# Optimization experiments

Measured on AMD Instinct MI355X. Metric: run time of the kernel, lower is better.

Reference implementation:

```python
import jax, jax.numpy as jnp
import numpy as np
from jax import lax

HEADS = 4
DSTATE = 8
DHALF = 64
DTRANK = 8
GRID_SIZE = 5
SPLINE_ORDER = 3


def _ln(x, g, b, eps=1e-5):
    mu = x.mean(-1, keepdims=True)
    v = ((x - mu) ** 2).mean(-1, keepdims=True)
    return (x - mu) / jnp.sqrt(v + eps) * g + b


def _make_grid(in_f):
    h = 2.0 / GRID_SIZE
    g = jnp.arange(-SPLINE_ORDER, GRID_SIZE + SPLINE_ORDER + 1, dtype=jnp.float32) * h - 1.0
    return jnp.tile(g[None, :], (in_f, 1))  # (in, grid+2k+1)


def _b_splines(x, grid):
    # x: (batch, in); grid: (in, G+2k+1) -> (batch, in, G+k)
    xe = x[:, :, None]
    bases = ((xe >= grid[:, :-1]) & (xe < grid[:, 1:])).astype(x.dtype)
    for k in range(1, SPLINE_ORDER + 1):
        bases = ((xe - grid[:, :-(k + 1)]) / (grid[:, k:-1] - grid[:, :-(k + 1)])) * bases[:, :, :-1] \
              + ((grid[:, k + 1:] - xe) / (grid[:, k + 1:] - grid[:, 1:-k])) * bases[:, :, 1:]
    return bases


def _kan_layer(x, bw, sw, sc, grid):
    base = jax.nn.silu(x) @ bw.T
    bs = _b_splines(x, grid)
    return base + jnp.einsum('bic,oic->bo', bs, sw * sc[:, :, None])


def _fkan(x, ng, nb, bw0, sw0, sc0, bw1, sw1, sc1):
    B, N, C = x.shape
    xf = _ln(x, ng, nb).reshape(B * N, C)
    h = _kan_layer(xf, bw0, sw0, sc0, _make_grid(C))
    y = _kan_layer(h, bw1, sw1, sc1, _make_grid(bw0.shape[0]))
    return y.reshape(B, N, C)


def _conv1x1(x, w, b):
    return jnp.einsum('bchw,oc->bohw', x, w[:, :, 0, 0]) + b[None, :, None, None]


def _dwconv2d(x, w, b):
    y = lax.conv_general_dilated(x, w, (1, 1), 'SAME', feature_group_count=x.shape[1],
                                 dimension_numbers=('NCHW', 'OIHW', 'NCHW'))
    return y + b[None, :, None, None]


def _dwconv1d(x, w):
    return lax.conv_general_dilated(x, w, (1,), 'SAME', feature_group_count=x.shape[1],
                                    dimension_numbers=('NCH', 'OIH', 'NCH'))


def _attention(x, temp, qkv_w, qkv_b, dw_w, dw_b, po_w, po_b):
    b, c, h, w = x.shape
    qkv = _dwconv2d(_conv1x1(x, qkv_w, qkv_b), dw_w, dw_b)
    q, k, v = jnp.split(qkv, 3, axis=1)
    rs = lambda t: t.reshape(b, HEADS, c // HEADS, h * w)
    q, k, v = rs(q), rs(k), rs(v)
    q = q / jnp.maximum(jnp.linalg.norm(q, axis=-1, keepdims=True), 1e-12)
    k = k / jnp.maximum(jnp.linalg.norm(k, axis=-1, keepdims=True), 1e-12)
    attn = jax.nn.softmax(jnp.einsum('bhcn,bhdn->bhcd', q, k) * temp, axis=-1)
    out = jnp.einsum('bhcd,bhdn->bhcn', attn, v).reshape(b, c, h, w)
    return _conv1x1(out, po_w, po_b)


def _mamba(x, in_w, xp_w, dt_w, dt_b, A_log, Dp, out_w, cx_w, cz_w):
    B, L, C = x.shape
    xz = x @ in_w.T                       # (B, L, d_inner)
    xc, zc = jnp.split(xz, 2, axis=-1)    # each (B, L, DHALF)
    xl = jax.nn.silu(_dwconv1d(xc.transpose(0, 2, 1), cx_w)).transpose(0, 2, 1)
    zl = jax.nn.silu(_dwconv1d(zc.transpose(0, 2, 1), cz_w)).transpose(0, 2, 1)
    x_dbl = xl @ xp_w.T                   # (B, L, dt_rank + 2*d_state)
    dt, Bm, Cm = jnp.split(x_dbl, [DTRANK, DTRANK + DSTATE], axis=-1)
    delta = jax.nn.softplus(dt @ dt_w.T + dt_b)   # (B, L, DHALF)
    A = -jnp.exp(A_log)                   # (DHALF, DSTATE)
    dA = jnp.exp(jnp.einsum('bld,dn->bldn', delta, A))
    dBu = delta[..., None] * Bm[:, :, None, :] * xl[..., None]

    def step(hst, inp):
        dA_t, dBu_t, C_t = inp
        hst = dA_t * hst + dBu_t
        return hst, jnp.einsum('bdn,bn->bd', hst, C_t)

    h0 = jnp.zeros((B, DHALF, DSTATE), x.dtype)
    _, ys = lax.scan(step, h0, (dA.transpose(1, 0, 2, 3), dBu.transpose(1, 0, 2, 3), Cm.transpose(1, 0, 2)))
    y = ys.transpose(1, 0, 2) + xl * Dp
    return jnp.concatenate([y, zl], axis=-1) @ out_w.T


def _forward(x5d, ln1_g, ln1_b, ln2_g, ln2_b, ln3_g, ln3_b, ln4_g, ln4_b,
             attn_temp, attn_qkv_w, attn_qkv_b, attn_dw_w, attn_dw_b, attn_po_w, attn_po_b,
             ffn1_ng, ffn1_nb, ffn1_bw0, ffn1_sw0, ffn1_sc0, ffn1_bw1, ffn1_sw1, ffn1_sc1,
             ffn2_ng, ffn2_nb, ffn2_bw0, ffn2_sw0, ffn2_sc0, ffn2_bw1, ffn2_sw1, ffn2_sc1,
             in_proj_w, x_proj_w, dt_proj_w, dt_proj_b, A_log, D_param, out_proj_w, conv_x_w, conv_z_w):
    B, C, Dd, H, W = x5d.shape
    N = Dd * H * W
    Hs = int(np.sqrt(N))
    x = x5d.reshape(B, C, N).transpose(0, 2, 1)   # (B, N, C)
    t2d = _ln(x, ln1_g, ln1_b).transpose(0, 2, 1).reshape(B, C, Hs, Hs)
    a = _attention(t2d, attn_temp, attn_qkv_w, attn_qkv_b, attn_dw_w, attn_dw_b, attn_po_w, attn_po_b)
    t = x + a.reshape(B, C, N).transpose(0, 2, 1)
    u = _fkan(_ln(t, ln2_g, ln2_b), ffn1_ng, ffn1_nb, ffn1_bw0, ffn1_sw0, ffn1_sc0, ffn1_bw1, ffn1_sw1, ffn1_sc1) + t
    x_tr = x + u
    m = _mamba(_ln(x_tr, ln3_g, ln3_b), in_proj_w, x_proj_w, dt_proj_w, dt_proj_b, A_log, D_param, out_proj_w, conv_x_w, conv_z_w) + x_tr
    n = _fkan(_ln(m, ln4_g, ln4_b), ffn2_ng, ffn2_nb, ffn2_bw0, ffn2_sw0, ffn2_sc0, ffn2_bw1, ffn2_sw1, ffn2_sc1) + m
    out = x_tr + n
    return out.transpose(0, 2, 1).reshape(B, C, Dd, H, W)


def setup_inputs():
    key = jax.random.key(0)
    ks = iter(jax.random.split(key, 48))
    f32 = jnp.float32

    def rn(shape, s=0.05):
        return jax.random.normal(next(ks), shape, f32) * s

    B, C, Dd, H, W = 2, 128, 1, 96, 96
    MLP = 512
    d = {}
    d['x5d'] = jax.random.normal(next(ks), (B, C, Dd, H, W), f32)
    for nm in ('ln1', 'ln2', 'ln3', 'ln4'):
        d[nm + '_g'] = jnp.ones((C,), f32)
        d[nm + '_b'] = jnp.zeros((C,), f32)
    d['attn_temp'] = jnp.ones((HEADS, 1, 1), f32)
    d['attn_qkv_w'] = rn((3 * C, C, 1, 1)); d['attn_qkv_b'] = jnp.zeros((3 * C,), f32)
    d['attn_dw_w'] = rn((3 * C, 1, 3, 3), 0.2); d['attn_dw_b'] = jnp.zeros((3 * C,), f32)
    d['attn_po_w'] = rn((C, C, 1, 1)); d['attn_po_b'] = jnp.zeros((C,), f32)
    for p in ('ffn1', 'ffn2'):
        d[p + '_ng'] = jnp.ones((C,), f32); d[p + '_nb'] = jnp.zeros((C,), f32)
        d[p + '_bw0'] = rn((MLP, C)); d[p + '_sw0'] = rn((MLP, C, GRID_SIZE + SPLINE_ORDER), 0.02); d[p + '_sc0'] = jnp.ones((MLP, C), f32)
        d[p + '_bw1'] = rn((C, MLP)); d[p + '_sw1'] = rn((C, MLP, GRID_SIZE + SPLINE_ORDER), 0.02); d[p + '_sc1'] = jnp.ones((C, MLP), f32)
    d['in_proj_w'] = rn((C, C))
    d['x_proj_w'] = rn((DTRANK + 2 * DSTATE, DHALF))
    std = DTRANK ** -0.5
    d['dt_proj_w'] = jax.random.uniform(next(ks), (DHALF, DTRANK), f32, -std, std)
    dt = jnp.exp(jax.random.uniform(next(ks), (DHALF,), f32) * (np.log(0.1) - np.log(0.001)) + np.log(0.001))
    dt = jnp.clip(dt, 1e-4, None)
    d['dt_proj_b'] = dt + jnp.log(-jnp.expm1(-dt))
    d['A_log'] = jnp.log(jnp.tile(jnp.arange(1, DSTATE + 1, dtype=f32)[None, :], (DHALF, 1)))
    d['D_param'] = jnp.ones((DHALF,), f32)
    d['out_proj_w'] = rn((C, C))
    d['conv_x_w'] = rn((DHALF, 1, 3), 0.2)
    d['conv_z_w'] = rn((DHALF, 1, 3), 0.2)
    return d


def reference(x5d, ln1_g, ln1_b, ln2_g, ln2_b, ln3_g, ln3_b, ln4_g, ln4_b,
              attn_temp, attn_qkv_w, attn_qkv_b, attn_dw_w, attn_dw_b, attn_po_w, attn_po_b,
              ffn1_ng, ffn1_nb, ffn1_bw0, ffn1_sw0, ffn1_sc0, ffn1_bw1, ffn1_sw1, ffn1_sc1,
              ffn2_ng, ffn2_nb, ffn2_bw0, ffn2_sw0, ffn2_sc0, ffn2_bw1, ffn2_sw1, ffn2_sc1,
              in_proj_w, x_proj_w, dt_proj_w, dt_proj_b, A_log, D_param, out_proj_w, conv_x_w, conv_z_w):
    return _forward(x5d, ln1_g, ln1_b, ln2_g, ln2_b, ln3_g, ln3_b, ln4_g, ln4_b,
                    attn_temp, attn_qkv_w, attn_qkv_b, attn_dw_w, attn_dw_b, attn_po_w, attn_po_b,
                    ffn1_ng, ffn1_nb, ffn1_bw0, ffn1_sw0, ffn1_sc0, ffn1_bw1, ffn1_sw1, ffn1_sc1,
                    ffn2_ng, ffn2_nb, ffn2_bw0, ffn2_sw0, ffn2_sc0, ffn2_bw1, ffn2_sw1, ffn2_sc1,
                    in_proj_w, x_proj_w, dt_proj_w, dt_proj_b, A_log, D_param, out_proj_w, conv_x_w, conv_z_w)
```

## Files before the change

kernel.cpp:

```cpp
#include <hip/hip_runtime.h>

typedef unsigned short u16;
typedef __attribute__((ext_vector_type(8))) short bh8;
typedef __attribute__((ext_vector_type(4))) float f4;

#define DI __device__ __forceinline__

DI u16 f2bf(float f){ unsigned u=__float_as_uint(f); u += 0x7fffu + ((u>>16)&1u); return (u16)(u>>16); }
DI float bf2f(u16 u){ return __uint_as_float(((unsigned)u)<<16); }
DI float silu_f(float x){ return x/(1.f+__expf(-x)); }

DI void gld16(const u16* g, u16* l){
  __builtin_amdgcn_global_load_lds((const __attribute__((address_space(1))) void*)g,
                                   (__attribute__((address_space(3))) void*)l, 16, 0, 0);
}

DI void bspline8(float x, float* v){
  float u = x*2.5f + 5.5f;
  #pragma unroll
  for (int j=0;j<8;j++){
    float a  = fabsf(u - (float)(j+2));
    float t1 = fmaxf(2.f-a, 0.f);
    float t2 = fmaxf(1.f-a, 0.f);
    v[j] = t1*t1*t1*(1.f/6.f) - t2*t2*t2*(2.f/3.f);
  }
}

template<int KAN_H, bool OUT_BF16>
__global__ __launch_bounds__(256, 4)
void gemm_kernel(const void* __restrict__ Asrc, const u16* __restrict__ Bt,
                 void* __restrict__ Cout, int M, int N, int K, int ktiles_per_z,
                 int split, const float* __restrict__ bias, const float* __restrict__ R1)
{
  __shared__ u16 sA[128*64];
  __shared__ u16 sB[128*64];
  const int m0 = blockIdx.y * 128;
  const int n0 = blockIdx.x * 128;
  const int ktiles = K >> 6;
  int kt0 = blockIdx.z * ktiles_per_z;
  int kt1 = kt0 + ktiles_per_z; if (kt1 > ktiles) kt1 = ktiles;
  const int t = threadIdx.x;
  const int wave = t >> 6, lane = t & 63;
  const int wm = wave & 1, wn = wave >> 1;
  const int lr = lane & 15, lq = lane >> 4;
  const int lr8 = lane >> 3, lc8 = lane & 7;
  const int swz8 = lc8 ^ lr8;
  f4 acc[4][4];
  f4 z4 = {0.f,0.f,0.f,0.f};
  #pragma unroll
  for (int i=0;i<4;i++)
    #pragma unroll
    for (int j=0;j<4;j++) acc[i][j]=z4;

  for (int kt = kt0; kt < kt1; ++kt) {
    int k0 = kt << 6;
    {
      const u16* Bp = Bt + (size_t)n0 * K + k0;
      #pragma unroll
      for (int it=0; it<4; ++it) {
        int r = it*32 + wave*8;
        gld16(Bp + (size_t)(r + lr8) * K + swz8*8, &sB[r*64]);
      }
    }
    if (KAN_H == 0) {
      const u16* Ap = (const u16*)Asrc + (size_t)m0 * K + k0;
      #pragma unroll
      for (int it=0; it<4; ++it) {
        int r = it*32 + wave*8;
        gld16(Ap + (size_t)(r + lr8) * K + swz8*8, &sA[r*64]);
      }
    } else {
      const u16* hsrc = (const u16*)Asrc;
      if (k0 < KAN_H) {
        #pragma unroll
        for (int it=0; it<4; ++it) {
          int chunk = t + it*256;
          int r = chunk >> 3, ck = chunk & 7;
          const u16* src = hsrc + (size_t)(m0+r)*KAN_H + k0 + ck*8;
          ushort4 a = *(const ushort4*)src;
          ushort4 b2 = *(const ushort4*)(src+4);
          alignas(16) u16 o[8];
          o[0]=f2bf(silu_f(bf2f(a.x))); o[1]=f2bf(silu_f(bf2f(a.y)));
          o[2]=f2bf(silu_f(bf2f(a.z))); o[3]=f2bf(silu_f(bf2f(a.w)));
          o[4]=f2bf(silu_f(bf2f(b2.x))); o[5]=f2bf(silu_f(bf2f(b2.y)));
          o[6]=f2bf(silu_f(bf2f(b2.z))); o[7]=f2bf(silu_f(bf2f(b2.w)));
          *(float4*)(&sA[r*64 + (ck ^ (r&7))*8]) = *(const float4*)o;
        }
      } else {
        int i0 = (k0 - KAN_H) >> 3;
        #pragma unroll
        for (int it=0; it<4; ++it) {
          int chunk = t + it*256;
          int r = chunk >> 3, ii = chunk & 7;
          float x = bf2f(hsrc[(size_t)(m0+r)*KAN_H + i0 + ii]);
          float w[8];
          bspline8(x, w);
          alignas(16) u16 o[8];
          #pragma unroll
          for (int j=0;j<8;j++) o[j]=f2bf(w[j]);
          *(float4*)(&sA[r*64 + (ii ^ (r&7))*8]) = *(const float4*)o;
        }
      }
    }
    __syncthreads();
    #pragma unroll
    for (int kk=0; kk<64; kk+=32) {
      const int c0 = kk >> 3;
      bh8 af[4], bfr[4];
      #pragma unroll
      for (int i=0;i<4;i++) {
        int row = wm*64 + i*16 + lr;
        af[i] = *(const bh8*)(&sA[row*64 + ((c0+lq) ^ (row&7))*8]);
      }
      #pragma unroll
      for (int j=0;j<4;j++) {
        int row = wn*64 + j*16 + lr;
        bfr[j] = *(const bh8*)(&sB[row*64 + ((c0+lq) ^ (row&7))*8]);
      }
      #pragma unroll
      for (int i=0;i<4;i++)
        #pragma unroll
        for (int j=0;j<4;j++)
          acc[i][j] = __builtin_amdgcn_mfma_f32_16x16x32_bf16(af[i], bfr[j], acc[i][j], 0, 0, 0);
    }
    __syncthreads();
  }
  float* Cf = (float*)Cout;
  if (!OUT_BF16 && split) Cf += (size_t)blockIdx.z * M * N;
  u16* Cb = (u16*)Cout;
  #pragma unroll
  for (int i=0;i<4;i++) {
    int row = m0 + wm*64 + i*16 + lq*4;
    #pragma unroll
    for (int j=0;j<4;j++) {
      int col = n0 + wn*64 + j*16 + lr;
      float bv = bias ? bias[col] : 0.f;
      #pragma unroll
      for (int r4=0;r4<4;r4++) {
        size_t idx = (size_t)(row + r4) * N + col;
        float v = acc[i][j][r4] + bv;
        if (OUT_BF16) {
          Cb[idx] = f2bf(v);
        } else {
          if (R1) v += R1[idx];
          Cf[idx] = v;
        }
      }
    }
  }
}

__global__ __launch_bounds__(256) void k_ln1_trans(const float* __restrict__ x5d,
    float* __restrict__ x_t, u16* __restrict__ ln1_t,
    const float* __restrict__ g, const float* __restrict__ bv)
{
  __shared__ float tile[128*65];
  __shared__ float red_s[256], red_q[256];
  __shared__ float st_mu[64], st_rs[64];
  int b = blockIdx.y, n0 = blockIdx.x * 64;
  int j = threadIdx.x & 63, part = threadIdx.x >> 6;
  for (int cc=0; cc<32; ++cc) {
    int c = part*32 + cc;
    tile[c*65 + j] = x5d[((size_t)b*128 + c)*9216 + n0 + j];
  }
  __syncthreads();
  float s=0.f, s2=0.f;
  for (int cc=0; cc<32; ++cc) {
    float v = tile[(part*32+cc)*65 + j];
    s += v; s2 += v*v;
  }
  red_s[threadIdx.x]=s; red_q[threadIdx.x]=s2;
  __syncthreads();
  if (threadIdx.x < 64) {
    int jj = threadIdx.x;
    float ts = red_s[jj]+red_s[jj+64]+red_s[jj+128]+red_s[jj+192];
    float tq = red_q[jj]+red_q[jj+64]+red_q[jj+128]+red_q[jj+192];
    float mu = ts*(1.f/128.f);
    st_mu[jj]=mu;
    st_rs[jj]=rsqrtf(tq*(1.f/128.f) - mu*mu + 1e-5f);
  }
  __syncthreads();
  for (int it=0; it<32; ++it) {
    int idx = threadIdx.x + it*256;
    int tok = idx >> 7, c = idx & 127;
    float v = tile[c*65 + tok];
    size_t a = ((size_t)b*9216 + n0 + tok)*128 + c;
    x_t[a] = v;
    ln1_t[a] = f2bf((v - st_mu[tok])*st_rs[tok]*g[c] + bv[c]);
  }
}

__global__ void k_ln_bf16(const float* __restrict__ in, u16* __restrict__ out,
                          const float* __restrict__ g, const float* __restrict__ bv)
{
  int tok = blockIdx.x*4 + (threadIdx.x>>6);
  int lane = threadIdx.x & 63;
  const float* row = in + (size_t)tok*128;
  float v0=row[lane], v1=row[lane+64];
  float s=v0+v1, s2=v0*v0+v1*v1;
  #pragma unroll
  for (int o=1;o<64;o<<=1){ s += __shfl_xor(s,o); s2 += __shfl_xor(s2,o); }
  float mu=s*(1.f/128.f);
  float rs=rsqrtf(s2*(1.f/128.f)-mu*mu+1e-5f);
  u16* orow = out + (size_t)tok*128;
  orow[lane]    = f2bf((v0-mu)*rs*g[lane]+bv[lane]);
  orow[lane+64] = f2bf((v1-mu)*rs*g[lane+64]+bv[lane+64]);
}

__global__ void k_ln_double_expand(const float* __restrict__ in, u16* __restrict__ A1,
    const float* __restrict__ g1, const float* __restrict__ b1,
    const float* __restrict__ g2, const float* __restrict__ b2)
{
  int tok = blockIdx.x*4 + (threadIdx.x>>6);
  int lane = threadIdx.x & 63;
  const float* row = in + (size_t)tok*128;
  float v0=row[lane], v1=row[lane+64];
  float s=v0+v1, s2=v0*v0+v1*v1;
  #pragma unroll
  for (int o=1;o<64;o<<=1){ s += __shfl_xor(s,o); s2 += __shfl_xor(s2,o); }
  float mu=s*(1.f/128.f);
  float rs=rsqrtf(s2*(1.f/128.f)-mu*mu+1e-5f);
  float y0=(v0-mu)*rs*g1[lane]+b1[lane];
  float y1=(v1-mu)*rs*g1[lane+64]+b1[lane+64];
  s=y0+y1; s2=y0*y0+y1*y1;
  #pragma unroll
  for (int o=1;o<64;o<<=1){ s += __shfl_xor(s,o); s2 += __shfl_xor(s2,o); }
  mu=s*(1.f/128.f);
  rs=rsqrtf(s2*(1.f/128.f)-mu*mu+1e-5f);
  y0=(y0-mu)*rs*g2[lane]+b2[lane];
  y1=(y1-mu)*rs*g2[lane+64]+b2[lane+64];
  u16* arow = A1 + (size_t)tok*1152;
  arow[lane]    = f2bf(silu_f(y0));
  arow[lane+64] = f2bf(silu_f(y1));
  float w[8]; alignas(16) u16 o8[8];
  bspline8(y0, w);
  #pragma unroll
  for (int j=0;j<8;j++) o8[j]=f2bf(w[j]);
  *(float4*)(&arow[128 + lane*8]) = *(const float4*)o8;
  bspline8(y1, w);
  #pragma unroll
  for (int j=0;j<8;j++) o8[j]=f2bf(w[j]);
  *(float4*)(&arow[128 + (lane+64)*8]) = *(const float4*)o8;
}

__global__ __launch_bounds__(256) void k_dwconv(const u16* __restrict__ qkv_t,
    u16* __restrict__ qkvd, const float* __restrict__ dw_w, const float* __restrict__ dw_b)
{
  __shared__ float lt[100*68];
  int tile = blockIdx.x; int th=(tile/12)*8, tw=(tile%12)*8;
  int cg = blockIdx.y, b = blockIdx.z;
  int t = threadIdx.x;
  for (int pp=0; pp<7; ++pp) {
    int pos = pp*16 + (t>>4);
    if (pos < 100) {
      int ih = th + pos/10 - 1, iw = tw + pos%10 - 1;
      int c4 = (t & 15)*4;
      float4 v = make_float4(0.f,0.f,0.f,0.f);
      if (ih>=0 && ih<96 && iw>=0 && iw<96) {
        ushort4 raw = *(const ushort4*)&qkv_t[(((size_t)b*9216) + ih*96 + iw)*384 + cg*64 + c4];
        v = make_float4(bf2f(raw.x), bf2f(raw.y), bf2f(raw.z), bf2f(raw.w));
      }
      *(float4*)&lt[pos*68 + c4] = v;
    }
  }
  __syncthreads();
  int ch = t & 63, gch = cg*64 + ch;
  float w[9];
  #pragma unroll
  for (int k=0;k<9;k++) w[k]=dw_w[gch*9+k];
  float bias = dw_b[gch];
  for (int pp=0; pp<16; ++pp) {
    int pos = (t>>6) + pp*4;
    int oh = pos>>3, ow = pos&7;
    float acc = bias;
    #pragma unroll
    for (int di=0; di<3; ++di)
      #pragma unroll
      for (int dj=0; dj<3; ++dj)
        acc += lt[((oh+di)*10 + ow+dj)*68 + ch] * w[di*3+dj];
    qkvd[(((size_t)b*9216) + (th+oh)*96 + tw+ow)*384 + gch] = f2bf(acc);
  }
}

__global__ void k_normsum(const u16* __restrict__ qkvd, float* __restrict__ ss)
{
  int b = blockIdx.y, n0 = blockIdx.x*128;
  int c = threadIdx.x;
  float acc=0.f;
  for (int i=0;i<128;++i){
    float v = bf2f(qkvd[((size_t)b*9216 + n0+i)*384 + c]);
    acc += v*v;
  }
  atomicAdd(&ss[b*256 + c], acc);
}

__global__ __launch_bounds__(256) void k_qk(const u16* __restrict__ qkvd,
    const float* __restrict__ ss, float* __restrict__ S)
{
  __shared__ float ql[128][32];
  __shared__ float kl[128][32];
  int nc=blockIdx.x, h=blockIdx.y, b=blockIdx.z;
  int t = threadIdx.x;
  int r = t>>1, half = t&1;
  size_t rowa = ((size_t)b*9216 + nc*128 + r)*384 + (half?128:0) + h*32;
  #pragma unroll
  for (int cc=0; cc<32; ++cc) {
    float v = bf2f(qkvd[rowa + cc]);
    if (half) kl[r][cc]=v; else ql[r][cc]=v;
  }
  __syncthreads();
  int i0 = (t>>4)*2, j0 = (t&15)*2;
  float a00=0.f,a01=0.f,a10=0.f,a11=0.f;
  for (int n=0;n<128;++n){
    float2 qv = *(const float2*)&ql[n][i0];
    float2 kv = *(const float2*)&kl[n][j0];
    a00 += qv.x*kv.x; a01 += qv.x*kv.y;
    a10 += qv.y*kv.x; a11 += qv.y*kv.y;
  }
  const float* ssb = ss + b*256;
  float rq0 = 1.f/fmaxf(sqrtf(ssb[h*32+i0]),1e-12f);
  float rq1 = 1.f/fmaxf(sqrtf(ssb[h*32+i0+1]),1e-12f);
  float rk0 = 1.f/fmaxf(sqrtf(ssb[128+h*32+j0]),1e-12f);
  float rk1 = 1.f/fmaxf(sqrtf(ssb[128+h*32+j0+1]),1e-12f);
  float* Sp = S + ((size_t)(b*4+h))*1024;
  atomicAdd(&Sp[i0*32+j0],     a00*rq0*rk0);
  atomicAdd(&Sp[i0*32+j0+1],   a01*rq0*rk1);
  atomicAdd(&Sp[(i0+1)*32+j0], a10*rq1*rk0);
  atomicAdd(&Sp[(i0+1)*32+j0+1], a11*rq1*rk1);
}

__global__ void k_softmax(const float* __restrict__ S, float* __restrict__ attnP,
                          const float* __restrict__ temp)
{
  int bh = blockIdx.x; int h = bh & 3;
  int i = threadIdx.x;
  const float* row = S + (size_t)bh*1024 + i*32;
  float tp = temp[h];
  float vals[32]; float mx = -1e30f;
  #pragma unroll
  for (int j=0;j<32;++j){ float v=row[j]*tp; vals[j]=v; mx=fmaxf(mx,v); }
  float sum=0.f;
  #pragma unroll
  for (int j=0;j<32;++j){ vals[j]=__expf(vals[j]-mx); sum+=vals[j]; }
  float inv=1.f/sum;
  float* out = attnP + (size_t)bh*1024 + i*32;
  #pragma unroll
  for (int j=0;j<32;++j) out[j]=vals[j]*inv;
}

__global__ __launch_bounds__(256) void k_av(const u16* __restrict__ qkvd,
    const float* __restrict__ attnP, u16* __restrict__ attnout)
{
  __shared__ float at[1024];
  int b=blockIdx.z, h=blockIdx.y;
  int n = blockIdx.x*256 + threadIdx.x;
  #pragma unroll
  for (int it=0;it<4;++it)
    at[threadIdx.x + it*256] = attnP[((size_t)(b*4+h))*1024 + threadIdx.x + it*256];
  __syncthreads();
  const u16* vrow = &qkvd[((size_t)b*9216 + n)*384 + 256 + h*32];
  float acc[32];
  #pragma unroll
  for (int i=0;i<32;++i) acc[i]=0.f;
  #pragma unroll 4
  for (int j=0;j<32;++j){
    float vj = bf2f(vrow[j]);
    #pragma unroll
    for (int i=0;i<32;++i) acc[i] += at[i*32+j]*vj;
  }
  u16* orow = &attnout[((size_t)b*9216 + n)*128 + h*32];
  #pragma unroll
  for (int i=0;i<32;++i) orow[i] = f2bf(acc[i]);
}

__global__ void k_reduce4(const float4* __restrict__ P, const float4* __restrict__ R1,
                          const float4* __restrict__ R2, float4* __restrict__ o, int n4)
{
  int i = blockIdx.x*256 + threadIdx.x;
  if (i<n4){
    float4 a=P[i], b=P[i+n4], c=P[i+2*n4], d=P[i+3*n4], r=R1[i], s=R2[i];
    o[i]=make_float4(a.x+b.x+c.x+d.x+r.x+s.x, a.y+b.y+c.y+d.y+r.y+s.y,
                     a.z+b.z+c.z+d.z+r.z+s.z, a.w+b.w+c.w+d.w+r.w+s.w);
  }
}

__global__ void k_zero(float* p, int n){ int i=blockIdx.x*256+threadIdx.x; if(i<n)p[i]=0.f; }
__global__ void k_f2bf_copy(const float* __restrict__ in, u16* __restrict__ out, int n){
  int i=blockIdx.x*256+threadIdx.x; if(i<n) out[i]=f2bf(in[i]);
}

__global__ __launch_bounds__(256) void k_mamba_pre(const float* __restrict__ xz,
    float* __restrict__ xl, float* __restrict__ delta,
    float* __restrict__ Bm, float* __restrict__ Cm, u16* __restrict__ A_out,
    const float* __restrict__ cxw, const float* __restrict__ czw,
    const float* __restrict__ xpw, const float* __restrict__ dtw, const float* __restrict__ dtb)
{
  __shared__ float xls[4][64];
  __shared__ float xds[4][24];
  int w = threadIdx.x>>6;
  int tok = blockIdx.x*4 + w;
  int lane = threadIdx.x & 63;
  int l = tok % 9216;
  size_t base = (size_t)tok*128;
  float xm1 = (l>0)?     xz[base-128+lane]    : 0.f;
  float x0  =            xz[base+lane];
  float xp1 = (l<9215)?  xz[base+128+lane]    : 0.f;
  float zm1 = (l>0)?     xz[base-128+64+lane] : 0.f;
  float z0  =            xz[base+64+lane];
  float zp1 = (l<9215)?  xz[base+128+64+lane] : 0.f;
  float xc = silu_f(cxw[lane*3]*xm1 + cxw[lane*3+1]*x0 + cxw[lane*3+2]*xp1);
  float zc = silu_f(czw[lane*3]*zm1 + czw[lane*3+1]*z0 + czw[lane*3+2]*zp1);
  xl[(size_t)tok*64+lane] = xc;
  A_out[(size_t)tok*128 + 64 + lane] = f2bf(zc);
  xls[w][lane] = xc;
  __syncthreads();
  if (lane < 24) {
    float s=0.f;
    #pragma unroll 8
    for (int c=0;c<64;++c) s += xls[w][c]*xpw[lane*64+c];
    xds[w][lane]=s;
  }
  __syncthreads();
  float dacc = dtb[lane];
  #pragma unroll
  for (int r=0;r<8;++r) dacc += xds[w][r]*dtw[lane*8+r];
  delta[(size_t)tok*64+lane] = (dacc>20.f)? dacc : log1pf(__expf(dacc));
  if (lane<8)       Bm[(size_t)tok*8+lane]   = xds[w][8+lane];
  else if (lane<16) Cm[(size_t)tok*8+lane-8] = xds[w][16+lane-8];
}

__global__ __launch_bounds__(512) void k_scan1(const float* __restrict__ delta,
    const float* __restrict__ Bm, const float* __restrict__ xl,
    const float* __restrict__ Aneg, float* __restrict__ cP, float* __restrict__ cS)
{
  int b=blockIdx.y, ch=blockIdx.x;
  int t=threadIdx.x; int d=t>>3, n=t&7;
  float An = Aneg[d*8+n];
  float P=1.f, S=0.f;
  int l0 = ch*96;
  #pragma unroll 8
  for (int i=0;i<96;++i){
    size_t s = (size_t)b*9216 + l0+i;
    float del = delta[s*64+d];
    float a = __expf(del*An);
    float dbu = del * Bm[s*8+n] * xl[s*64+d];
    P *= a; S = fmaf(a,S,dbu);
  }
  size_t o = ((size_t)(b*96+ch))*512 + t;
  cP[o]=P; cS[o]=S;
}

__global__ __launch_bounds__(512) void k_scan2(const float* __restrict__ cP,
    const float* __restrict__ cS, float* __restrict__ cI)
{
  int b=blockIdx.x; int t=threadIdx.x;
  float carry=0.f;
  #pragma unroll 4
  for (int c=0;c<96;++c){
    size_t o = ((size_t)(b*96+c))*512 + t;
    cI[o]=carry;
    carry = fmaf(cP[o], carry, cS[o]);
  }
}

__global__ __launch_bounds__(512) void k_scan3(const float* __restrict__ delta,
    const float* __restrict__ Bm, const float* __restrict__ Cm,
    const float* __restrict__ xl, const float* __restrict__ Aneg,
    const float* __restrict__ Dp, const float* __restrict__ cI, u16* __restrict__ A_out)
{
  int b=blockIdx.y, ch=blockIdx.x;
  int t=threadIdx.x; int d=t>>3, n=t&7;
  float An = Aneg[d*8+n];
  float h = cI[((size_t)(b*96+ch))*512 + t];
  float Dd = Dp[d];
  int l0 = ch*96;
  #pragma unroll 4
  for (int i=0;i<96;++i){
    size_t s = (size_t)b*9216 + l0+i;
    float del = delta[s*64+d];
    float a = __expf(del*An);
    float xv = xl[s*64+d];
    h = fmaf(a, h, del * Bm[s*8+n] * xv);
    float contrib = h * Cm[s*8+n];
    contrib += __shfl_xor(contrib,1);
    contrib += __shfl_xor(contrib,2);
    contrib += __shfl_xor(contrib,4);
    if (n==0) A_out[s*128 + d] = f2bf(contrib + xv*Dd);
  }
}

__global__ __launch_bounds__(256) void k_transpose_out(const float* __restrict__ sfin,
                                                       float* __restrict__ out)
{
  __shared__ float tile[128*65];
  int b=blockIdx.y, n0=blockIdx.x*64;
  for (int it=0;it<32;++it){
    int idx = threadIdx.x + it*256;
    int tok = idx>>7, c = idx&127;
    tile[c*65+tok] = sfin[((size_t)b*9216 + n0+tok)*128 + c];
  }
  __syncthreads();
  int j = threadIdx.x & 63, part = threadIdx.x>>6;
  for (int cc=0;cc<32;++cc){
    int c = part*32+cc;
    out[((size_t)b*128 + c)*9216 + n0 + j] = tile[c*65 + j];
  }
}

__global__ void k_pack_w1t(const float* __restrict__ bw0, const float* __restrict__ sw0,
                           const float* __restrict__ sc0, u16* __restrict__ W1t)
{
  int idx = blockIdx.x*256 + threadIdx.x;
  if (idx >= 512*1152) return;
  int o = idx/1152, k = idx%1152;
  float v;
  if (k < 128) v = bw0[o*128+k];
  else { int i=(k-128)>>3, c=(k-128)&7; v = sw0[(o*128+i)*8+c]*sc0[o*128+i]; }
  W1t[idx]=f2bf(v);
}
__global__ void k_pack_w2t(const float* __restrict__ bw1, const float* __restrict__ sw1,
                           const float* __restrict__ sc1, u16* __restrict__ W2t)
{
  int idx = blockIdx.x*256 + threadIdx.x;
  if (idx >= 128*4608) return;
  int o = idx/4608, k = idx%4608;
  float v;
  if (k < 512) v = bw1[o*512+k];
  else { int i=(k-512)>>3, c=(k-512)&7; v = sw1[(o*512+i)*8+c]*sc1[o*512+i]; }
  W2t[idx]=f2bf(v);
}
__global__ void k_prep_aneg(const float* __restrict__ A_log, float* __restrict__ Aneg){
  int i=threadIdx.x; if (i<512) Aneg[i] = -__expf(A_log[i]);
}

extern "C" void kernel_launch(void* const* d_in, const int* in_sizes, int n_in,
                              void* d_out, int out_size, void* d_ws, size_t ws_size,
                              hipStream_t stream)
{
  (void)in_sizes; (void)n_in; (void)out_size; (void)ws_size;
  const float* x5d   =(const float*)d_in[0];
  const float* ln1_g =(const float*)d_in[1];
  const float* ln1_b =(const float*)d_in[2];
  const float* ln2_g =(const float*)d_in[3];
  const float* ln2_b =(const float*)d_in[4];
  const float* ln3_g =(const float*)d_in[5];
  const float* ln3_b =(const float*)d_in[6];
  const float* ln4_g =(const float*)d_in[7];
  const float* ln4_b =(const float*)d_in[8];
  const float* temp  =(const float*)d_in[9];
  const float* qkv_w =(const float*)d_in[10];
  const float* qkv_b =(const float*)d_in[11];
  const float* dw_w  =(const float*)d_in[12];
  const float* dw_b  =(const float*)d_in[13];
  const float* po_w  =(const float*)d_in[14];
  const float* po_b  =(const float*)d_in[15];
  const float* f1_ng =(const float*)d_in[16];
  const float* f1_nb =(const float*)d_in[17];
  const float* f1_bw0=(const float*)d_in[18];
  const float* f1_sw0=(const float*)d_in[19];
  const float* f1_sc0=(const float*)d_in[20];
  const float* f1_bw1=(const float*)d_in[21];
  const float* f1_sw1=(const float*)d_in[22];
  const float* f1_sc1=(const float*)d_in[23];
  const float* f2_ng =(const float*)d_in[24];
  const float* f2_nb =(const float*)d_in[25];
  const float* f2_bw0=(const float*)d_in[26];
  const float* f2_sw0=(const float*)d_in[27];
  const float* f2_sc0=(const float*)d_in[28];
  const float* f2_bw1=(const float*)d_in[29];
  const float* f2_sw1=(const float*)d_in[30];
  const float* f2_sc1=(const float*)d_in[31];
  const float* in_w  =(const float*)d_in[32];
  const float* xp_w  =(const float*)d_in[33];
  const float* dt_w  =(const float*)d_in[34];
  const float* dt_b  =(const float*)d_in[35];
  const float* A_log =(const float*)d_in[36];
  const float* Dp    =(const float*)d_in[37];
  const float* out_w =(const float*)d_in[38];
  const float* cx_w  =(const float*)d_in[39];
  const float* cz_w  =(const float*)d_in[40];
  float* out = (float*)d_out;

  const size_t T = 18432;
  char* wsb = (char*)d_ws;
  size_t off = 0;
  auto alloc = [&](size_t bytes)->void* {
    void* p = wsb + off; off += (bytes + 255) & ~(size_t)255; return p;
  };
  float* x_t    = (float*)alloc(T*128*4);
  char*  scrA   = (char*) alloc(38*1024*1024);
  float* ssS    = (float*)alloc((512+8192+8192)*4);
  float* t_t    = (float*)alloc(T*128*4);
  u16*   A1     = (u16*)  alloc(T*1152*2);
  u16*   hbuf   = (u16*)  alloc(T*512*2);
  float* xtr    = (float*)alloc(T*128*4);
  u16*   xm     = (u16*)  alloc(T*128*2);
  float* xl     = (float*)alloc(T*64*4);
  float* delta  = (float*)alloc(T*64*4);
  float* Bm     = (float*)alloc(T*8*4);
  float* Cm     = (float*)alloc(T*8*4);
  u16*   A_out  = (u16*)  alloc(T*128*2);
  float* cP     = (float*)alloc(2*96*512*4);
  float* cS     = (float*)alloc(2*96*512*4);
  float* cI     = (float*)alloc(2*96*512*4);
  float* sfin   = (float*)alloc(T*128*4);
  u16* qkvw_bf  = (u16*)alloc(384*128*2);
  u16* pow_bf   = (u16*)alloc(128*128*2);
  u16* inw_bf   = (u16*)alloc(128*128*2);
  u16* outw_bf  = (u16*)alloc(128*128*2);
  u16* W1t_a    = (u16*)alloc(512*1152*2);
  u16* W2t_a    = (u16*)alloc(128*4608*2);
  u16* W1t_b    = (u16*)alloc(512*1152*2);
  u16* W2t_b    = (u16*)alloc(128*4608*2);
  float* Aneg   = (float*)alloc(512*4);
  float* ss = ssS;
  float* S  = ssS + 512;
  float* attnP = ssS + 512 + 8192;
  u16*   ln1_t  = (u16*)(scrA);
  u16*   qkv_tb = (u16*)(scrA + 4718592);
  u16*   qkvd   = (u16*)(scrA + 4718592 + 14155776);
  u16*   attnout= (u16*)(scrA + 4718592 + 2*14155776);
  float* part   = (float*)scrA;
  float* xz     = (float*)scrA;
  float* m_t    = t_t;

  k_pack_w1t<<<2304,256,0,stream>>>(f1_bw0, f1_sw0, f1_sc0, W1t_a);
  k_pack_w1t<<<2304,256,0,stream>>>(f2_bw0, f2_sw0, f2_sc0, W1t_b);
  k_pack_w2t<<<2304,256,0,stream>>>(f1_bw1, f1_sw1, f1_sc1, W2t_a);
  k_pack_w2t<<<2304,256,0,stream>>>(f2_bw1, f2_sw1, f2_sc1, W2t_b);
  k_f2bf_copy<<<192,256,0,stream>>>(qkv_w, qkvw_bf, 384*128);
  k_f2bf_copy<<<64,256,0,stream>>>(po_w,  pow_bf, 128*128);
  k_f2bf_copy<<<64,256,0,stream>>>(in_w,  inw_bf, 128*128);
  k_f2bf_copy<<<64,256,0,stream>>>(out_w, outw_bf, 128*128);
  k_prep_aneg<<<1,512,0,stream>>>(A_log, Aneg);
  k_zero<<<34,256,0,stream>>>(ssS, 512+8192);

  k_ln1_trans<<<dim3(144,2),256,0,stream>>>(x5d, x_t, ln1_t, ln1_g, ln1_b);
  gemm_kernel<0,true><<<dim3(3,144,1),256,0,stream>>>(ln1_t, qkvw_bf, qkv_tb,
      18432, 384, 128, 2, 0, qkv_b, nullptr);
  k_dwconv<<<dim3(144,6,2),256,0,stream>>>(qkv_tb, qkvd, dw_w, dw_b);
  k_normsum<<<dim3(72,2),256,0,stream>>>(qkvd, ss);
  k_qk<<<dim3(72,4,2),256,0,stream>>>(qkvd, ss, S);
  k_softmax<<<8,32,0,stream>>>(S, attnP, temp);
  k_av<<<dim3(36,4,2),256,0,stream>>>(qkvd, attnP, attnout);
  gemm_kernel<0,false><<<dim3(1,144,1),256,0,stream>>>(attnout, pow_bf, t_t,
      18432, 128, 128, 2, 0, po_b, x_t);

  k_ln_double_expand<<<4608,256,0,stream>>>(t_t, A1, ln2_g, ln2_b, f1_ng, f1_nb);
  gemm_kernel<0,true><<<dim3(4,144,1),256,0,stream>>>(A1, W1t_a, hbuf,
      18432, 512, 1152, 18, 0, nullptr, nullptr);
  gemm_kernel<512,false><<<dim3(1,144,4),256,0,stream>>>(hbuf, W2t_a, part,
      18432, 128, 4608, 18, 1, nullptr, nullptr);
  k_reduce4<<<2304,256,0,stream>>>((const float4*)part, (const float4*)t_t,
      (const float4*)x_t, (float4*)xtr, (int)(T*128/4));

  k_ln_bf16<<<4608,256,0,stream>>>(xtr, xm, ln3_g, ln3_b);
  gemm_kernel<0,false><<<dim3(1,144,1),256,0,stream>>>(xm, inw_bf, xz,
      18432, 128, 128, 2, 0, nullptr, nullptr);
  k_mamba_pre<<<4608,256,0,stream>>>(xz, xl, delta, Bm, Cm, A_out,
      cx_w, cz_w, xp_w, dt_w, dt_b);
  k_scan1<<<dim3(96,2),512,0,stream>>>(delta, Bm, xl, Aneg, cP, cS);
  k_scan2<<<2,512,0,stream>>>(cP, cS, cI);
  k_scan3<<<dim3(96,2),512,0,stream>>>(delta, Bm, Cm, xl, Aneg, Dp, cI, A_out);
  gemm_kernel<0,false><<<dim3(1,144,1),256,0,stream>>>(A_out, outw_bf, m_t,
      18432, 128, 128, 2, 0, nullptr, xtr);

  k_ln_double_expand<<<4608,256,0,stream>>>(m_t, A1, ln4_g, ln4_b, f2_ng, f2_nb);
  gemm_kernel<0,true><<<dim3(4,144,1),256,0,stream>>>(A1, W1t_b, hbuf,
      18432, 512, 1152, 18, 0, nullptr, nullptr);
  gemm_kernel<512,false><<<dim3(1,144,4),256,0,stream>>>(hbuf, W2t_b, part,
      18432, 128, 4608, 18, 1, nullptr, nullptr);
  k_reduce4<<<2304,256,0,stream>>>((const float4*)part, (const float4*)m_t,
      (const float4*)xtr, (float4*)sfin, (int)(T*128/4));

  k_transpose_out<<<dim3(144,2),256,0,stream>>>(sfin, out);
}
```

Before: 593.5 us.

## Halve GEMM M-tile, sparsify spline basis, fuse reduce+LN and prep kernels

The GEMM tile shrinks from 128x128 to 64x128 and the grid's M dimension doubles from 144 to 288 blocks, giving more blocks across the GPU's CUs. The B-spline A-tile fill now computes only the 4 nonzero cubic weights, placed at their knot offset after zeroing the row, instead of evaluating all 8 bases. The residual reduction is fused with LayerNorm3, and the small weight-conversion, Aneg and zeroing kernels merge into one prep launch. The trade-off is less B-tile reuse per block, since each B tile loaded into shared memory now serves only 64 rows of A.

```diff
diff --git a/kernel.cpp b/kernel.cpp
--- a/kernel.cpp
+++ b/kernel.cpp
@@ -28,29 +28,26 @@
 
 template<int KAN_H, bool OUT_BF16>
 __global__ __launch_bounds__(256, 4)
-void gemm_kernel(const void* __restrict__ Asrc, const u16* __restrict__ Bt,
-                 void* __restrict__ Cout, int M, int N, int K, int ktiles_per_z,
-                 int split, const float* __restrict__ bias, const float* __restrict__ R1)
-{
-  __shared__ u16 sA[128*64];
+void gemm64(const void* __restrict__ Asrc, const u16* __restrict__ Bt,
+            void* __restrict__ Cout, int M, int N, int K, int ktiles_per_z,
+            int split, const float* __restrict__ bias, const float* __restrict__ R1)
+{
+  __shared__ u16 sA[64*64 + 8];
   __shared__ u16 sB[128*64];
-  const int m0 = blockIdx.y * 128;
+  const int m0 = blockIdx.y * 64;
   const int n0 = blockIdx.x * 128;
   const int ktiles = K >> 6;
   int kt0 = blockIdx.z * ktiles_per_z;
   int kt1 = kt0 + ktiles_per_z; if (kt1 > ktiles) kt1 = ktiles;
   const int t = threadIdx.x;
   const int wave = t >> 6, lane = t & 63;
-  const int wm = wave & 1, wn = wave >> 1;
   const int lr = lane & 15, lq = lane >> 4;
   const int lr8 = lane >> 3, lc8 = lane & 7;
   const int swz8 = lc8 ^ lr8;
-  f4 acc[4][4];
+  f4 acc[4][2];
   f4 z4 = {0.f,0.f,0.f,0.f};
   #pragma unroll
-  for (int i=0;i<4;i++)
-    #pragma unroll
-    for (int j=0;j<4;j++) acc[i][j]=z4;
+  for (int i=0;i<4;i++){ acc[i][0]=z4; acc[i][1]=z4; }
 
   for (int kt = kt0; kt < kt1; ++kt) {
     int k0 = kt << 6;
@@ -65,7 +62,7 @@
     if (KAN_H == 0) {
       const u16* Ap = (const u16*)Asrc + (size_t)m0 * K + k0;
       #pragma unroll
-      for (int it=0; it<4; ++it) {
+      for (int it=0; it<2; ++it) {
         int r = it*32 + wave*8;
         gld16(Ap + (size_t)(r + lr8) * K + swz8*8, &sA[r*64]);
       }
@@ -73,7 +70,7 @@
       const u16* hsrc = (const u16*)Asrc;
       if (k0 < KAN_H) {
         #pragma unroll
-        for (int it=0; it<4; ++it) {
+        for (int it=0; it<2; ++it) {
           int chunk = t + it*256;
           int r = chunk >> 3, ck = chunk & 7;
           const u16* src = hsrc + (size_t)(m0+r)*KAN_H + k0 + ck*8;
@@ -88,39 +85,55 @@
         }
       } else {
         int i0 = (k0 - KAN_H) >> 3;
+        const float4 zf4 = make_float4(0.f,0.f,0.f,0.f);
         #pragma unroll
-        for (int it=0; it<4; ++it) {
-          int chunk = t + it*256;
-          int r = chunk >> 3, ii = chunk & 7;
+        for (int it=0; it<2; ++it) {
+          int pair = t + it*256;
+          int r = pair >> 3, ii = pair & 7;
+          int base = r*64 + (ii ^ (r&7))*8;
+          *(float4*)(&sA[base]) = zf4;
           float x = bf2f(hsrc[(size_t)(m0+r)*KAN_H + i0 + ii]);
-          float w[8];
-          bspline8(x, w);
-          alignas(16) u16 o[8];
+          float u = x*2.5f + 5.5f;
+          bool valid = (u >= 0.f) & (u < 11.f);
+          float uc = fminf(fmaxf(u, 0.f), 10.999f);
+          int m = (int)uc;
+          float tt = uc - (float)m;
+          float omt = 1.f - tt, t2 = tt*tt, t3 = t2*tt;
+          float w0 = omt*omt*omt*(1.f/6.f);
+          float w3 = t3*(1.f/6.f);
+          float w1 = 0.5f*t3 - t2 + (2.f/3.f);
+          float w2 = 1.f - w0 - w1 - w3;
+          float ws[4] = {w0, w1, w2, w3};
+          int c0 = m - 3;
           #pragma unroll
-          for (int j=0;j<8;j++) o[j]=f2bf(w[j]);
-          *(float4*)(&sA[r*64 + (ii ^ (r&7))*8]) = *(const float4*)o;
+          for (int j=0;j<4;j++){
+            int c = c0 + j;
+            bool ok = valid & ((unsigned)c < 8u);
+            int off = ok ? (base + c) : (64*64);
+            sA[off] = f2bf(ws[j]);
+          }
         }
       }
     }
     __syncthreads();
     #pragma unroll
     for (int kk=0; kk<64; kk+=32) {
-      const int c0 = kk >> 3;
-      bh8 af[4], bfr[4];
+      const int c0k = kk >> 3;
+      bh8 af[4], bfr[2];
       #pragma unroll
       for (int i=0;i<4;i++) {
-        int row = wm*64 + i*16 + lr;
-        af[i] = *(const bh8*)(&sA[row*64 + ((c0+lq) ^ (row&7))*8]);
+        int row = i*16 + lr;
+        af[i] = *(const bh8*)(&sA[row*64 + ((c0k+lq) ^ (row&7))*8]);
       }
       #pragma unroll
-      for (int j=0;j<4;j++) {
-        int row = wn*64 + j*16 + lr;
-        bfr[j] = *(const bh8*)(&sB[row*64 + ((c0+lq) ^ (row&7))*8]);
+      for (int j=0;j<2;j++) {
+        int row = wave*32 + j*16 + lr;
+        bfr[j] = *(const bh8*)(&sB[row*64 + ((c0k+lq) ^ (row&7))*8]);
       }
       #pragma unroll
       for (int i=0;i<4;i++)
         #pragma unroll
-        for (int j=0;j<4;j++)
+        for (int j=0;j<2;j++)
           acc[i][j] = __builtin_amdgcn_mfma_f32_16x16x32_bf16(af[i], bfr[j], acc[i][j], 0, 0, 0);
     }
     __syncthreads();
@@ -130,10 +143,10 @@
   u16* Cb = (u16*)Cout;
   #pragma unroll
   for (int i=0;i<4;i++) {
-    int row = m0 + wm*64 + i*16 + lq*4;
+    int row = m0 + i*16 + lq*4;
     #pragma unroll
-    for (int j=0;j<4;j++) {
-      int col = n0 + wn*64 + j*16 + lr;
+    for (int j=0;j<2;j++) {
+      int col = n0 + wave*32 + j*16 + lr;
       float bv = bias ? bias[col] : 0.f;
       #pragma unroll
       for (int r4=0;r4<4;r4++) {
@@ -188,23 +201,6 @@
     x_t[a] = v;
     ln1_t[a] = f2bf((v - st_mu[tok])*st_rs[tok]*g[c] + bv[c]);
   }
-}
-
-__global__ void k_ln_bf16(const float* __restrict__ in, u16* __restrict__ out,
-                          const float* __restrict__ g, const float* __restrict__ bv)
-{
-  int tok = blockIdx.x*4 + (threadIdx.x>>6);
-  int lane = threadIdx.x & 63;
-  const float* row = in + (size_t)tok*128;
-  float v0=row[lane], v1=row[lane+64];
-  float s=v0+v1, s2=v0*v0+v1*v1;
-  #pragma unroll
-  for (int o=1;o<64;o<<=1){ s += __shfl_xor(s,o); s2 += __shfl_xor(s2,o); }
-  float mu=s*(1.f/128.f);
-  float rs=rsqrtf(s2*(1.f/128.f)-mu*mu+1e-5f);
-  u16* orow = out + (size_t)tok*128;
-  orow[lane]    = f2bf((v0-mu)*rs*g[lane]+bv[lane]);
-  orow[lane+64] = f2bf((v1-mu)*rs*g[lane+64]+bv[lane+64]);
 }
 
 __global__ void k_ln_double_expand(const float* __restrict__ in, u16* __restrict__ A1,
@@ -384,9 +380,50 @@
   }
 }
 
-__global__ void k_zero(float* p, int n){ int i=blockIdx.x*256+threadIdx.x; if(i<n)p[i]=0.f; }
-__global__ void k_f2bf_copy(const float* __restrict__ in, u16* __restrict__ out, int n){
-  int i=blockIdx.x*256+threadIdx.x; if(i<n) out[i]=f2bf(in[i]);
+__global__ void k_reduce4_ln(const float4* __restrict__ P, const float4* __restrict__ R1,
+    const float4* __restrict__ R2, float4* __restrict__ xtr, u16* __restrict__ xm,
+    const float* __restrict__ g, const float* __restrict__ bv, int n4)
+{
+  int i = blockIdx.x*256 + threadIdx.x;
+  int q = i & 31;
+  float4 a=P[i], b=P[i+n4], c=P[i+2*n4], d=P[i+3*n4], r=R1[i], s=R2[i];
+  float4 v=make_float4(a.x+b.x+c.x+d.x+r.x+s.x, a.y+b.y+c.y+d.y+r.y+s.y,
+                       a.z+b.z+c.z+d.z+r.z+s.z, a.w+b.w+c.w+d.w+r.w+s.w);
+  xtr[i]=v;
+  float s1 = v.x+v.y+v.z+v.w;
+  float s2 = v.x*v.x+v.y*v.y+v.z*v.z+v.w*v.w;
+  #pragma unroll
+  for (int o=1;o<32;o<<=1){ s1 += __shfl_xor(s1,o); s2 += __shfl_xor(s2,o); }
+  float mu = s1*(1.f/128.f);
+  float rs = rsqrtf(s2*(1.f/128.f)-mu*mu+1e-5f);
+  float4 g4 = *(const float4*)(g + q*4);
+  float4 b4 = *(const float4*)(bv + q*4);
+  ushort4 o4;
+  o4.x = f2bf((v.x-mu)*rs*g4.x + b4.x);
+  o4.y = f2bf((v.y-mu)*rs*g4.y + b4.y);
+  o4.z = f2bf((v.z-mu)*rs*g4.z + b4.z);
+  o4.w = f2bf((v.w-mu)*rs*g4.w + b4.w);
+  ((ushort4*)xm)[i] = o4;
+}
+
+__global__ void k_prep(const float* __restrict__ qkv_w, const float* __restrict__ po_w,
+    const float* __restrict__ in_w, const float* __restrict__ out_w,
+    const float* __restrict__ A_log, u16* __restrict__ qkvw_bf, u16* __restrict__ pow_bf,
+    u16* __restrict__ inw_bf, u16* __restrict__ outw_bf, float* __restrict__ Aneg,
+    float* __restrict__ zbuf, int nz)
+{
+  int i = blockIdx.x*256 + threadIdx.x;
+  if (i < 49152) { qkvw_bf[i] = f2bf(qkv_w[i]); return; }
+  i -= 49152;
+  if (i < 16384) { pow_bf[i] = f2bf(po_w[i]); return; }
+  i -= 16384;
+  if (i < 16384) { inw_bf[i] = f2bf(in_w[i]); return; }
+  i -= 16384;
+  if (i < 16384) { outw_bf[i] = f2bf(out_w[i]); return; }
+  i -= 16384;
+  if (i < 512) { Aneg[i] = -__expf(A_log[i]); return; }
+  i -= 512;
+  if (i < nz) zbuf[i] = 0.f;
 }
 
 __global__ __launch_bounds__(256) void k_mamba_pre(const float* __restrict__ xz,
@@ -528,9 +565,6 @@
   if (k < 512) v = bw1[o*512+k];
   else { int i=(k-512)>>3, c=(k-512)&7; v = sw1[(o*512+i)*8+c]*sc1[o*512+i]; }
   W2t[idx]=f2bf(v);
-}
-__global__ void k_prep_aneg(const float* __restrict__ A_log, float* __restrict__ Aneg){
-  int i=threadIdx.x; if (i<512) Aneg[i] = -__expf(A_log[i]);
 }
 
 extern "C" void kernel_launch(void* const* d_in, const int* in_sizes, int n_in,
@@ -628,47 +662,42 @@
   k_pack_w1t<<<2304,256,0,stream>>>(f2_bw0, f2_sw0, f2_sc0, W1t_b);
   k_pack_w2t<<<2304,256,0,stream>>>(f1_bw1, f1_sw1, f1_sc1, W2t_a);
   k_pack_w2t<<<2304,256,0,stream>>>(f2_bw1, f2_sw1, f2_sc1, W2t_b);
-  k_f2bf_copy<<<192,256,0,stream>>>(qkv_w, qkvw_bf, 384*128);
-  k_f2bf_copy<<<64,256,0,stream>>>(po_w,  pow_bf, 128*128);
-  k_f2bf_copy<<<64,256,0,stream>>>(in_w,  inw_bf, 128*128);
-  k_f2bf_copy<<<64,256,0,stream>>>(out_w, outw_bf, 128*128);
-  k_prep_aneg<<<1,512,0,stream>>>(A_log, Aneg);
-  k_zero<<<34,256,0,stream>>>(ssS, 512+8192);
+  k_prep<<<420,256,0,stream>>>(qkv_w, po_w, in_w, out_w, A_log,
+      qkvw_bf, pow_bf, inw_bf, outw_bf, Aneg, ssS, 512+8192);
 
   k_ln1_trans<<<dim3(144,2),256,0,stream>>>(x5d, x_t, ln1_t, ln1_g, ln1_b);
-  gemm_kernel<0,true><<<dim3(3,144,1),256,0,stream>>>(ln1_t, qkvw_bf, qkv_tb,
+  gemm64<0,true><<<dim3(3,288,1),256,0,stream>>>(ln1_t, qkvw_bf, qkv_tb,
       18432, 384, 128, 2, 0, qkv_b, nullptr);
   k_dwconv<<<dim3(144,6,2),256,0,stream>>>(qkv_tb, qkvd, dw_w, dw_b);
   k_normsum<<<dim3(72,2),256,0,stream>>>(qkvd, ss);
   k_qk<<<dim3(72,4,2),256,0,stream>>>(qkvd, ss, S);
   k_softmax<<<8,32,0,stream>>>(S, attnP, temp);
   k_av<<<dim3(36,4,2),256,0,stream>>>(qkvd, attnP, attnout);
-  gemm_kernel<0,false><<<dim3(1,144,1),256,0,stream>>>(attnout, pow_bf, t_t,
+  gemm64<0,false><<<dim3(1,288,1),256,0,stream>>>(attnout, pow_bf, t_t,
       18432, 128, 128, 2, 0, po_b, x_t);
 
   k_ln_double_expand<<<4608,256,0,stream>>>(t_t, A1, ln2_g, ln2_b, f1_ng, f1_nb);
-  gemm_kernel<0,true><<<dim3(4,144,1),256,0,stream>>>(A1, W1t_a, hbuf,
+  gemm64<0,true><<<dim3(4,288,1),256,0,stream>>>(A1, W1t_a, hbuf,
       18432, 512, 1152, 18, 0, nullptr, nullptr);
-  gemm_kernel<512,false><<<dim3(1,144,4),256,0,stream>>>(hbuf, W2t_a, part,
+  gemm64<512,false><<<dim3(1,288,4),256,0,stream>>>(hbuf, W2t_a, part,
       18432, 128, 4608, 18, 1, nullptr, nullptr);
-  k_reduce4<<<2304,256,0,stream>>>((const float4*)part, (const float4*)t_t,
-      (const float4*)x_t, (float4*)xtr, (int)(T*128/4));
-
-  k_ln_bf16<<<4608,256,0,stream>>>(xtr, xm, ln3_g, ln3_b);
-  gemm_kernel<0,false><<<dim3(1,144,1),256,0,stream>>>(xm, inw_bf, xz,
+  k_reduce4_ln<<<2304,256,0,stream>>>((const float4*)part, (const float4*)t_t,
+      (const float4*)x_t, (float4*)xtr, xm, ln3_g, ln3_b, (int)(T*128/4));
+
+  gemm64<0,false><<<dim3(1,288,1),256,0,stream>>>(xm, inw_bf, xz,
       18432, 128, 128, 2, 0, nullptr, nullptr);
   k_mamba_pre<<<4608,256,0,stream>>>(xz, xl, delta, Bm, Cm, A_out,
       cx_w, cz_w, xp_w, dt_w, dt_b);
   k_scan1<<<dim3(96,2),512,0,stream>>>(delta, Bm, xl, Aneg, cP, cS);
   k_scan2<<<2,512,0,stream>>>(cP, cS, cI);
   k_scan3<<<dim3(96,2),512,0,stream>>>(delta, Bm, Cm, xl, Aneg, Dp, cI, A_out);
-  gemm_kernel<0,false><<<dim3(1,144,1),256,0,stream>>>(A_out, outw_bf, m_t,
+  gemm64<0,false><<<dim3(1,288,1),256,0,stream>>>(A_out, outw_bf, m_t,
       18432, 128, 128, 2, 0, nullptr, xtr);
 
   k_ln_double_expand<<<4608,256,0,stream>>>(m_t, A1, ln4_g, ln4_b, f2_ng, f2_nb);
-  gemm_kernel<0,true><<<dim3(4,144,1),256,0,stream>>>(A1, W1t_b, hbuf,
+  gemm64<0,true><<<dim3(4,288,1),256,0,stream>>>(A1, W1t_b, hbuf,
       18432, 512, 1152, 18, 0, nullptr, nullptr);
-  gemm_kernel<512,false><<<dim3(1,144,4),256,0,stream>>>(hbuf, W2t_b, part,
+  gemm64<512,false><<<dim3(1,288,4),256,0,stream>>>(hbuf, W2t_b, part,
       18432, 128, 4608, 18, 1, nullptr, nullptr);
   k_reduce4<<<2304,256,0,stream>>>((const float4*)part, (const float4*)m_t,
       (const float4*)xtr, (float4*)sfin, (int)(T*128/4));
```

Result: faster. 530.4 us (-10.6%).
